# Performance work log

Measured on AMD Instinct MI355X. Metric: run time of the kernel, lower is better.

Reference implementation:

```python
import jax, jax.numpy as jnp
import numpy as np

N = 50000
E = 800000
IN_DIM = 128
OUT_DIM = 64


def setup_inputs() -> dict:
    key = jax.random.key(0)
    ks = jax.random.split(key, 6)
    adj = jax.random.randint(ks[0], (2, E), 0, N)
    h = jax.random.normal(ks[1], (N, IN_DIM), dtype=jnp.float32)
    # fc: Linear(in_dim, out_dim) -> weight [out_dim, in_dim], bias [out_dim]
    W_fc = jax.random.normal(ks[2], (OUT_DIM, IN_DIM), dtype=jnp.float32) * (1.0 / np.sqrt(IN_DIM))
    b_fc = jnp.zeros((OUT_DIM,), dtype=jnp.float32)
    # attn_fc: Linear(2*out_dim, 1) -> weight [1, 2*out_dim], bias [1]
    W_att = jax.random.normal(ks[3], (1, 2 * OUT_DIM), dtype=jnp.float32) * (1.0 / np.sqrt(2 * OUT_DIM))
    b_att = jnp.zeros((1,), dtype=jnp.float32)
    return {"adj": adj, "h": h, "W_fc": W_fc, "b_fc": b_fc, "W_att": W_att, "b_att": b_att}


def reference(adj, h, W_fc, b_fc, W_att, b_att):
    # z = fc(h): [N, out_dim]
    z = h @ W_fc.T + b_fc
    src = adj[0]
    dst = adj[1]
    z_src = z[src]  # [E, out_dim]
    z_dst = z[dst]  # [E, out_dim]
    # attn_fc(cat(z_src, z_dst)) == z_src @ W1 + z_dst @ W2 + b; avoid explicit concat split
    w1 = W_att[0, :OUT_DIM]
    w2 = W_att[0, OUT_DIM:]
    att_logit = z_src @ w1 + z_dst @ w2 + b_att[0]  # [E]
    att_edge = jax.nn.leaky_relu(att_logit, negative_slope=0.01)[:, None]  # [E, 1]
    # scatter-add weighted source features to destination nodes
    out = jax.ops.segment_sum(z_src * att_edge, dst, num_segments=N)  # [N, out_dim]
    return out
```

## Files before the change

### kernel.cpp

```cpp
#include <hip/hip_runtime.h>
#include <hip/hip_bf16.h>

#define N_NODES 50000
#define E_EDGES 800000
#define IN_DIM  128
#define OUT_DIM 64
#define MTILES  (N_NODES / 16)
#define CAP     40
#define OVF_CAP 16384
#define CSTRIDE 8
#define NBLK_FC 782
#define NBLK_SC 2048
#define SLICE_N 6250
#define EPB     3125

static_assert(N_NODES % 16 == 0, "16-row MFMA tiles");
static_assert(N_NODES < 65536, "node ids packed as ushort");
static_assert(8 * SLICE_N == N_NODES, "slices partition dst space");
static_assert(256 * EPB == E_EDGES, "ranks partition edges");


typedef __attribute__((ext_vector_type(8))) short bf16x8;
typedef __attribute__((ext_vector_type(4))) float f32x4;
typedef __attribute__((ext_vector_type(8))) unsigned short u16x8;

__device__ __forceinline__ unsigned short f32_to_bf16_rne(float f) {
    unsigned u = __float_as_uint(f);
    return (unsigned short)((u + 0x7FFFu + ((u >> 16) & 1u)) >> 16);
}
__device__ __forceinline__ float bf16_to_f32(unsigned short s) {
    return __uint_as_float(((unsigned)s) << 16);
}

__global__ __launch_bounds__(256) void gat_fc_scatter(
    const float* __restrict__ h,
    const float* __restrict__ Wfc,
    const float* __restrict__ bfc,
    const float* __restrict__ Watt,
    const float* __restrict__ batt,
    const int*   __restrict__ adj,
    unsigned short* __restrict__ z16,
    float* __restrict__ s1,
    float* __restrict__ s2,
    int*   __restrict__ cntp,
    unsigned short* __restrict__ srcs,
    int*   __restrict__ ovf)
{
    __shared__ short Wlds[OUT_DIM][IN_DIM + 8];

    if (blockIdx.x < NBLK_FC) {
        for (int i = threadIdx.x; i < OUT_DIM * IN_DIM; i += 256) {
            const int o = i >> 7;
            const int k = i & 127;
            Wlds[o][k] = (short)f32_to_bf16_rne(Wfc[i]);
        }
        __syncthreads();

        const int lane  = threadIdx.x & 63;
        const int c     = lane & 15;
        const int q     = lane >> 4;
        const int mtile = blockIdx.x * 4 + (threadIdx.x >> 6);
        if (mtile >= MTILES) return;
        const int n0 = mtile * 16;

        bf16x8 B[4][4];
        #pragma unroll
        for (int t = 0; t < 4; ++t)
            #pragma unroll
            for (int f = 0; f < 4; ++f)
                B[t][f] = *(const bf16x8*)&Wlds[f * 16 + c][t * 32 + q * 8];

        f32x4 acc[4] = {{0,0,0,0},{0,0,0,0},{0,0,0,0},{0,0,0,0}};

        const float* arow = h + (size_t)(n0 + c) * IN_DIM + q * 8;
        #pragma unroll
        for (int t = 0; t < 4; ++t) {
            float4 x0 = *(const float4*)(arow + t * 32);
            float4 x1 = *(const float4*)(arow + t * 32 + 4);
            bf16x8 a;
            a[0] = (short)f32_to_bf16_rne(x0.x);
            a[1] = (short)f32_to_bf16_rne(x0.y);
            a[2] = (short)f32_to_bf16_rne(x0.z);
            a[3] = (short)f32_to_bf16_rne(x0.w);
            a[4] = (short)f32_to_bf16_rne(x1.x);
            a[5] = (short)f32_to_bf16_rne(x1.y);
            a[6] = (short)f32_to_bf16_rne(x1.z);
            a[7] = (short)f32_to_bf16_rne(x1.w);
            #pragma unroll
            for (int f = 0; f < 4; ++f)
                acc[f] = __builtin_amdgcn_mfma_f32_16x16x32_bf16(a, B[t][f], acc[f], 0, 0, 0);
        }

        const float batt0 = batt[0];
        float w1c[4], w2c[4], bv[4];
        #pragma unroll
        for (int f = 0; f < 4; ++f) {
            w1c[f] = Watt[f * 16 + c];
            w2c[f] = Watt[OUT_DIM + f * 16 + c];
            bv[f]  = bfc[f * 16 + c];
        }
        float p1[4] = {0,0,0,0}, p2[4] = {0,0,0,0};
        #pragma unroll
        for (int f = 0; f < 4; ++f)
            #pragma unroll
            for (int r = 0; r < 4; ++r) {
                const float v = acc[f][r] + bv[f];
                z16[(size_t)(n0 + q * 4 + r) * OUT_DIM + f * 16 + c] = f32_to_bf16_rne(v);
                p1[r] += v * w1c[f];
                p2[r] += v * w2c[f];
            }
        #pragma unroll
        for (int r = 0; r < 4; ++r) {
            #pragma unroll
            for (int off = 1; off < 16; off <<= 1) {
                p1[r] += __shfl_xor(p1[r], off, 64);
                p2[r] += __shfl_xor(p2[r], off, 64);
            }
            if (c == 0) {
                s1[n0 + q * 4 + r] = p1[r];
                s2[n0 + q * 4 + r] = p2[r] + batt0;
            }
        }
    } else {
        const int k     = blockIdx.x - NBLK_FC;
        const unsigned slice = blockIdx.x & 7;
        const int rank  = k >> 3;
        const unsigned lo = slice * SLICE_N;
        const int e0 = rank * EPB;
        const int e1 = e0 + EPB;

        for (int e = e0 + (int)threadIdx.x; e < e1; e += 256) {
            const unsigned dst = (unsigned)adj[E_EDGES + e];
            if (dst - lo < (unsigned)SLICE_N) {
                const int src = adj[e];
                const int pos = atomicAdd(&cntp[(size_t)dst * CSTRIDE], 1);
                if (pos < CAP) {
                    srcs[(size_t)dst * CAP + pos] = (unsigned short)src;
                } else {
                    const int o = atomicAdd(&cntp[(size_t)N_NODES * CSTRIDE], 1);
                    if (o < OVF_CAP) ovf[o] = ((int)dst << 16) | src;
                }
            }
        }
    }
}

__global__ __launch_bounds__(256) void gat_gather(
    const int* __restrict__ cntp, const unsigned short* __restrict__ srcs,
    const int* __restrict__ ovf,
    const float* __restrict__ s1, const float* __restrict__ s2,
    const unsigned short* __restrict__ z16,
    float* __restrict__ out)
{
    const int lane = threadIdx.x & 63;
    const int c    = lane & 7;
    const int q    = lane >> 3;
    const int n    = blockIdx.x * 4 + (threadIdx.x >> 6);
    if (n >= N_NODES) return;

    const int m = min(cntp[(size_t)n * CSTRIDE], CAP);
    const float s2n = s2[n];
    const unsigned short* row = srcs + (size_t)n * CAP;

    float acc[8] = {0,0,0,0,0,0,0,0};
    int j = 0;
    for (; j + 8 <= m; j += 8) {
        const int src = row[j + q];
        float a = s1[src] + s2n;
        a = (a > 0.f) ? a : 0.01f * a;
        const u16x8 zz = *(const u16x8*)&z16[(size_t)src * OUT_DIM + 8 * c];
        #pragma unroll
        for (int t = 0; t < 8; ++t) acc[t] += a * bf16_to_f32(zz[t]);
    }
    if (q < m - j) {
        const int src = row[j + q];
        float a = s1[src] + s2n;
        a = (a > 0.f) ? a : 0.01f * a;
        const u16x8 zz = *(const u16x8*)&z16[(size_t)src * OUT_DIM + 8 * c];
        #pragma unroll
        for (int t = 0; t < 8; ++t) acc[t] += a * bf16_to_f32(zz[t]);
    }

    const int novf = min(cntp[(size_t)N_NODES * CSTRIDE], OVF_CAP);
    for (int base = 0; base < novf; base += 8) {
        const int idx = base + q;
        int packed = (idx < novf) ? ovf[idx] : -1;
        const bool valid = (idx < novf) && ((packed >> 16) == n);
        const int src = valid ? (packed & 0xFFFF) : 0;
        float a = s1[src] + s2n;
        a = (a > 0.f) ? a : 0.01f * a;
        a = valid ? a : 0.f;
        const u16x8 zz = *(const u16x8*)&z16[(size_t)src * OUT_DIM + 8 * c];
        #pragma unroll
        for (int t = 0; t < 8; ++t) acc[t] += a * bf16_to_f32(zz[t]);
    }

    #pragma unroll
    for (int t = 0; t < 8; ++t) {
        acc[t] += __shfl_xor(acc[t], 8, 64);
        acc[t] += __shfl_xor(acc[t], 16, 64);
        acc[t] += __shfl_xor(acc[t], 32, 64);
    }

    if (q == 0) {
        float4 lo = make_float4(acc[0], acc[1], acc[2], acc[3]);
        float4 hi = make_float4(acc[4], acc[5], acc[6], acc[7]);
        *(float4*)&out[(size_t)n * OUT_DIM + 8 * c]     = lo;
        *(float4*)&out[(size_t)n * OUT_DIM + 8 * c + 4] = hi;
    }
}

extern "C" void kernel_launch(void* const* d_in, const int* in_sizes, int n_in,
                              void* d_out, int out_size, void* d_ws, size_t ws_size,
                              hipStream_t stream)
{
    const int*   adj  = (const int*)  d_in[0];
    const float* h    = (const float*)d_in[1];
    const float* Wfc  = (const float*)d_in[2];
    const float* bfc  = (const float*)d_in[3];
    const float* Watt = (const float*)d_in[4];
    const float* batt = (const float*)d_in[5];
    float* out = (float*)d_out;

    unsigned short* z16 = (unsigned short*)d_ws;
    float* s1   = (float*)(z16 + (size_t)N_NODES * OUT_DIM);
    float* s2   = s1 + N_NODES;
    int*   cntp = (int*)(s2 + N_NODES);
    int*   ovf  = cntp + ((size_t)N_NODES * CSTRIDE + CSTRIDE);
    unsigned short* srcs = (unsigned short*)(ovf + OVF_CAP);

    hipMemsetAsync(cntp, 0, ((size_t)N_NODES * CSTRIDE + CSTRIDE) * sizeof(int),
                   stream);

    gat_fc_scatter<<<NBLK_FC + NBLK_SC, 256, 0, stream>>>(
        h, Wfc, bfc, Watt, batt, adj, z16, s1, s2, cntp, srcs, ovf);
    gat_gather<<<(N_NODES + 3) / 4, 256, 0, stream>>>(cntp, srcs, ovf,
                                                      s1, s2, z16, out);
}
```

Baseline: 145.5 us.

## Replace per-node atomic slot lists with two-pass bucket sort into CSR

Edges are now grouped by destination with a two-level bucket sort. A pass-A phase counts each 256-node bucket in shared memory and reserves global bucket ranges with one atomic per bucket. A new binsort kernel then sorts each bucket locally in LDS and emits start and degree arrays. This removes the per-edge global atomics on strided counters, the 8x redundant edge reads across slices, and the large memset. The cost is an extra kernel launch, a 32-bit packed edge list that doubles the index bytes read in gather, and an overflow path if any bucket exceeds 6144 edges.

Result: faster. 134.9 us (-7.2%).

```diff
diff --git a/kernel.cpp b/kernel.cpp
--- a/kernel.cpp
+++ b/kernel.cpp
@@ -6,18 +6,17 @@
 #define IN_DIM  128
 #define OUT_DIM 64
 #define MTILES  (N_NODES / 16)
-#define CAP     40
+#define NB      196
+#define BCAP    6144
 #define OVF_CAP 16384
-#define CSTRIDE 8
 #define NBLK_FC 782
-#define NBLK_SC 2048
-#define SLICE_N 6250
-#define EPB     3125
+#define NBLK_SA 256
+#define EPA     3125
 
 static_assert(N_NODES % 16 == 0, "16-row MFMA tiles");
-static_assert(N_NODES < 65536, "node ids packed as ushort");
-static_assert(8 * SLICE_N == N_NODES, "slices partition dst space");
-static_assert(256 * EPB == E_EDGES, "ranks partition edges");
+static_assert(N_NODES < 65536, "node ids packed in 16 bits");
+static_assert(NBLK_SA * EPA == E_EDGES, "pass-A blocks partition edges");
+static_assert(NB * 256 >= N_NODES, "buckets cover dst space");
 
 
 typedef __attribute__((ext_vector_type(8))) short bf16x8;
@@ -42,11 +41,12 @@
     unsigned short* __restrict__ z16,
     float* __restrict__ s1,
     float* __restrict__ s2,
-    int*   __restrict__ cntp,
-    unsigned short* __restrict__ srcs,
-    int*   __restrict__ ovf)
+    int*      __restrict__ gcnt,
+    unsigned* __restrict__ coarse,
+    unsigned* __restrict__ ovf)
 {
     __shared__ short Wlds[OUT_DIM][IN_DIM + 8];
+    __shared__ int bcnt[NB], gbase[NB], lcur[NB];
 
     if (blockIdx.x < NBLK_FC) {
         for (int i = threadIdx.x; i < OUT_DIM * IN_DIM; i += 256) {
@@ -122,32 +122,85 @@
             }
         }
     } else {
-        const int k     = blockIdx.x - NBLK_FC;
-        const unsigned slice = blockIdx.x & 7;
-        const int rank  = k >> 3;
-        const unsigned lo = slice * SLICE_N;
-        const int e0 = rank * EPB;
-        const int e1 = e0 + EPB;
+        const int k  = blockIdx.x - NBLK_FC;
+        const int e0 = k * EPA, e1 = e0 + EPA;
+
+        for (int t = threadIdx.x; t < NB; t += 256) { bcnt[t] = 0; lcur[t] = 0; }
+        __syncthreads();
+
+        for (int e = e0 + (int)threadIdx.x; e < e1; e += 256)
+            atomicAdd(&bcnt[adj[E_EDGES + e] >> 8], 1);
+        __syncthreads();
+
+        for (int t = threadIdx.x; t < NB; t += 256)
+            gbase[t] = atomicAdd(&gcnt[t], bcnt[t]);
+        __syncthreads();
 
         for (int e = e0 + (int)threadIdx.x; e < e1; e += 256) {
             const unsigned dst = (unsigned)adj[E_EDGES + e];
-            if (dst - lo < (unsigned)SLICE_N) {
-                const int src = adj[e];
-                const int pos = atomicAdd(&cntp[(size_t)dst * CSTRIDE], 1);
-                if (pos < CAP) {
-                    srcs[(size_t)dst * CAP + pos] = (unsigned short)src;
-                } else {
-                    const int o = atomicAdd(&cntp[(size_t)N_NODES * CSTRIDE], 1);
-                    if (o < OVF_CAP) ovf[o] = ((int)dst << 16) | src;
-                }
-            }
-        }
+            const unsigned src = (unsigned)adj[e];
+            const int b = (int)(dst >> 8);
+            const int p = atomicAdd(&lcur[b], 1) + gbase[b];
+            const unsigned packed = (dst << 16) | src;
+            if (p < BCAP) {
+                coarse[(size_t)b * BCAP + p] = packed;
+            } else {
+                const int o = atomicAdd(&gcnt[NB], 1);
+                if (o < OVF_CAP) ovf[o] = packed;
+            }
+        }
+    }
+}
+
+__global__ __launch_bounds__(256) void gat_binsort(
+    unsigned* __restrict__ coarse,
+    const int* __restrict__ gcnt,
+    int* __restrict__ start, int* __restrict__ deg)
+{
+    __shared__ unsigned el[BCAP];
+    __shared__ int hist[256], sof[256], cur[256];
+    const int b  = blockIdx.x;
+    const int t  = threadIdx.x;
+    const int nb = min(gcnt[b], BCAP);
+
+    for (int i = t; i < nb; i += 256) el[i] = coarse[(size_t)b * BCAP + i];
+    hist[t] = 0;
+    __syncthreads();
+
+    for (int i = t; i < nb; i += 256)
+        atomicAdd(&hist[(el[i] >> 16) & 255], 1);
+    __syncthreads();
+
+    const int v = hist[t];
+    sof[t] = v;
+    __syncthreads();
+    #pragma unroll
+    for (int o = 1; o < 256; o <<= 1) {
+        const int add = (t >= o) ? sof[t - o] : 0;
+        __syncthreads();
+        sof[t] += add;
+        __syncthreads();
+    }
+    const int excl = sof[t] - v;
+    cur[t] = excl;
+    const int n = b * 256 + t;
+    if (n < N_NODES) {
+        start[n] = b * BCAP + excl;
+        deg[n]   = v;
+    }
+    __syncthreads();
+
+    for (int i = t; i < nb; i += 256) {
+        const unsigned e = el[i];
+        const int p = atomicAdd(&cur[(e >> 16) & 255], 1);
+        coarse[(size_t)b * BCAP + p] = e;
     }
 }
 
 __global__ __launch_bounds__(256) void gat_gather(
-    const int* __restrict__ cntp, const unsigned short* __restrict__ srcs,
-    const int* __restrict__ ovf,
+    const int* __restrict__ start, const int* __restrict__ deg,
+    const unsigned* __restrict__ coarse, const int* __restrict__ gcnt,
+    const unsigned* __restrict__ ovf,
     const float* __restrict__ s1, const float* __restrict__ s2,
     const unsigned short* __restrict__ z16,
     float* __restrict__ out)
@@ -158,14 +211,14 @@
     const int n    = blockIdx.x * 4 + (threadIdx.x >> 6);
     if (n >= N_NODES) return;
 
-    const int m = min(cntp[(size_t)n * CSTRIDE], CAP);
+    const int m  = deg[n];
+    const int jb = start[n];
     const float s2n = s2[n];
-    const unsigned short* row = srcs + (size_t)n * CAP;
 
     float acc[8] = {0,0,0,0,0,0,0,0};
     int j = 0;
     for (; j + 8 <= m; j += 8) {
-        const int src = row[j + q];
+        const int src = (int)(coarse[jb + j + q] & 0xFFFFu);
         float a = s1[src] + s2n;
         a = (a > 0.f) ? a : 0.01f * a;
         const u16x8 zz = *(const u16x8*)&z16[(size_t)src * OUT_DIM + 8 * c];
@@ -173,7 +226,7 @@
         for (int t = 0; t < 8; ++t) acc[t] += a * bf16_to_f32(zz[t]);
     }
     if (q < m - j) {
-        const int src = row[j + q];
+        const int src = (int)(coarse[jb + j + q] & 0xFFFFu);
         float a = s1[src] + s2n;
         a = (a > 0.f) ? a : 0.01f * a;
         const u16x8 zz = *(const u16x8*)&z16[(size_t)src * OUT_DIM + 8 * c];
@@ -181,12 +234,12 @@
         for (int t = 0; t < 8; ++t) acc[t] += a * bf16_to_f32(zz[t]);
     }
 
-    const int novf = min(cntp[(size_t)N_NODES * CSTRIDE], OVF_CAP);
+    const int novf = min(gcnt[NB], OVF_CAP);
     for (int base = 0; base < novf; base += 8) {
         const int idx = base + q;
-        int packed = (idx < novf) ? ovf[idx] : -1;
-        const bool valid = (idx < novf) && ((packed >> 16) == n);
-        const int src = valid ? (packed & 0xFFFF) : 0;
+        const unsigned packed = (idx < novf) ? ovf[idx] : 0xFFFFFFFFu;
+        const bool valid = (idx < novf) && ((packed >> 16) == (unsigned)n);
+        const int src = valid ? (int)(packed & 0xFFFFu) : 0;
         float a = s1[src] + s2n;
         a = (a > 0.f) ? a : 0.01f * a;
         a = valid ? a : 0.f;
@@ -223,17 +276,19 @@
     float* out = (float*)d_out;
 
     unsigned short* z16 = (unsigned short*)d_ws;
-    float* s1   = (float*)(z16 + (size_t)N_NODES * OUT_DIM);
-    float* s2   = s1 + N_NODES;
-    int*   cntp = (int*)(s2 + N_NODES);
-    int*   ovf  = cntp + ((size_t)N_NODES * CSTRIDE + CSTRIDE);
-    unsigned short* srcs = (unsigned short*)(ovf + OVF_CAP);
-
-    hipMemsetAsync(cntp, 0, ((size_t)N_NODES * CSTRIDE + CSTRIDE) * sizeof(int),
-                   stream);
-
-    gat_fc_scatter<<<NBLK_FC + NBLK_SC, 256, 0, stream>>>(
-        h, Wfc, bfc, Watt, batt, adj, z16, s1, s2, cntp, srcs, ovf);
-    gat_gather<<<(N_NODES + 3) / 4, 256, 0, stream>>>(cntp, srcs, ovf,
-                                                      s1, s2, z16, out);
-}
+    float* s1    = (float*)(z16 + (size_t)N_NODES * OUT_DIM);
+    float* s2    = s1 + N_NODES;
+    int*   start = (int*)(s2 + N_NODES);
+    int*   deg   = start + N_NODES;
+    int*   gcnt  = deg + N_NODES;
+    unsigned* ovf    = (unsigned*)(gcnt + NB + 1);
+    unsigned* coarse = ovf + OVF_CAP;
+
+    hipMemsetAsync(gcnt, 0, (NB + 1) * sizeof(int), stream);
+
+    gat_fc_scatter<<<NBLK_FC + NBLK_SA, 256, 0, stream>>>(
+        h, Wfc, bfc, Watt, batt, adj, z16, s1, s2, gcnt, coarse, ovf);
+    gat_binsort<<<NB, 256, 0, stream>>>(coarse, gcnt, start, deg);
+    gat_gather<<<(N_NODES + 3) / 4, 256, 0, stream>>>(
+        start, deg, coarse, gcnt, ovf, s1, s2, z16, out);
+}
```
